# Kernel tuning notes

Measured on AMD Instinct MI355X. Metric: run time of the kernel, lower is better.

## Reference

```python
import jax, jax.numpy as jnp
import numpy as np

WH, WW = 16, 16          # window size
S = WH * WW              # tokens per window = 256
B = 128                  # batch of windows
E = 1024                 # embed_dim
H = 16                   # num_heads
D = E // H               # head_dim = 64


def _swin_rel_index():
    # Swin-style relative position index, identical to the torch buffer construction
    coords = np.stack(np.meshgrid(np.arange(WH), np.arange(WW), indexing='ij'))  # [2,WH,WW]
    cf = coords.reshape(2, -1)                         # [2, S]
    rel = cf[:, :, None] - cf[:, None, :]              # [2, S, S]
    rel = rel.transpose(1, 2, 0).copy()                # [S, S, 2]
    rel[..., 0] += WH - 1
    rel[..., 1] += WW - 1
    rel[..., 0] *= 2 * WW - 1
    return rel.sum(-1).astype(np.int32)                # [S, S] in [0, (2WH-1)(2WW-1))


def setup_inputs() -> dict:
    key = jax.random.key(0)
    ks = jax.random.split(key, 6)
    x = jax.random.normal(ks[0], (B, S, E), dtype=jnp.float32)
    qkv_w = jax.random.normal(ks[1], (3 * E, E), dtype=jnp.float32) * 0.02
    qkv_b = jax.random.normal(ks[2], (3 * E,), dtype=jnp.float32) * 0.02
    out_w = jax.random.normal(ks[3], (E, E), dtype=jnp.float32) * 0.02
    out_b = jax.random.normal(ks[4], (E,), dtype=jnp.float32) * 0.02
    bias_table = jax.random.normal(ks[5], ((2 * WH - 1) * (2 * WW - 1), H), dtype=jnp.float32) * 0.02
    rel_index = jnp.asarray(_swin_rel_index())
    return {"x": x, "qkv_w": qkv_w, "qkv_b": qkv_b, "out_w": out_w,
            "out_b": out_b, "bias_table": bias_table, "rel_index": rel_index,
            "x_ignored_": 0, "x_ignored_1_": 0}


def reference(x, qkv_w, qkv_b, out_w, out_b, bias_table, rel_index, x_ignored_, x_ignored_1_):
    b, s, e = x.shape
    h = bias_table.shape[-1]
    d = e // h
    # fused QKV projection
    qkv = x @ qkv_w.T + qkv_b                          # [b, s, 3e]
    qkv = qkv.reshape(b, s, 3, h, d)
    q, k, v = qkv[:, :, 0], qkv[:, :, 1], qkv[:, :, 2]  # [b, s, h, d]
    scale = d ** -0.5
    # learned relative position bias, [h, s, s]
    bias = bias_table[rel_index.reshape(-1)].reshape(s, s, h).transpose(2, 0, 1)
    scores = jnp.einsum('bqhd,bkhd->bhqk', q, k) * scale + bias[None]
    attn = jax.nn.softmax(scores, axis=-1)
    ctx = jnp.einsum('bhqk,bkhd->bqhd', attn, v).reshape(b, s, e)
    return ctx @ out_w.T + out_b
```

## Files before the change

### kernel.cpp

```cpp
#include <hip/hip_runtime.h>
#include <stdint.h>

#define BB 128
#define SS 256
#define EE 1024
#define HH 16
#define DD 64
#define MM (BB*SS)

#define LOG2E 1.44269504088896f

typedef __attribute__((ext_vector_type(8))) short bf16x8;
typedef __attribute__((ext_vector_type(4))) float f32x4;

__device__ __forceinline__ unsigned short f2bf(float f) {
  union { float f; unsigned int u; } c; c.f = f;
  unsigned int u = c.u;
  u += 0x7fffu + ((u >> 16) & 1u);
  return (unsigned short)(u >> 16);
}

__device__ __forceinline__ float fast_exp2(float x) {
#if __has_builtin(__builtin_amdgcn_exp2f)
  return __builtin_amdgcn_exp2f(x);
#else
  return exp2f(x);
#endif
}

__device__ __forceinline__ float fast_rcp(float x) {
#if __has_builtin(__builtin_amdgcn_rcpf)
  return __builtin_amdgcn_rcpf(x);
#else
  return 1.0f / x;
#endif
}

__device__ __forceinline__ void gld16(const unsigned short* g, unsigned short* l) {
  __builtin_amdgcn_global_load_lds((__attribute__((address_space(1))) void*)(g),
                                   (__attribute__((address_space(3))) void*)(l), 16, 0, 0);
}

__global__ __launch_bounds__(256) void prep_kernel(const float4* __restrict__ x4,
                                                   const float4* __restrict__ qw,
                                                   const float4* __restrict__ ow,
                                                   const float* __restrict__ btab,
                                                   const int* __restrict__ ridx,
                                                   ushort4* __restrict__ xb,
                                                   ushort4* __restrict__ qwb,
                                                   ushort4* __restrict__ owb,
                                                   float* __restrict__ biasC) {
  const int NX = (MM * EE) / 4;
  const int NQ = (3 * EE * EE) / 4;
  const int NO = (EE * EE) / 4;
  const int NBIAS = HH * SS * SS;
  const int total = NX + NQ + NO + NBIAS;
  int stride = gridDim.x * blockDim.x;
  for (int i = blockIdx.x * blockDim.x + threadIdx.x; i < total; i += stride) {
    if (i < NX) {
      float4 v = x4[i];
      ushort4 r; r.x = f2bf(v.x); r.y = f2bf(v.y); r.z = f2bf(v.z); r.w = f2bf(v.w);
      xb[i] = r;
    } else if (i < NX + NQ) {
      int t = i - NX;
      float4 v = qw[t];
      ushort4 r; r.x = f2bf(v.x); r.y = f2bf(v.y); r.z = f2bf(v.z); r.w = f2bf(v.w);
      qwb[t] = r;
    } else if (i < NX + NQ + NO) {
      int t = i - (NX + NQ);
      float4 v = ow[t];
      ushort4 r; r.x = f2bf(v.x); r.y = f2bf(v.y); r.z = f2bf(v.z); r.w = f2bf(v.w);
      owb[t] = r;
    } else {
      int t = i - (NX + NQ + NO);
      int h   = t >> 16;
      int row = (t >> 8) & 255;
      int lo  = (t >> 4) & 15;
      int hi  = t & 15;
      int col = hi * 16 + lo;
      biasC[t] = btab[ridx[row * SS + col] * HH + h] * LOG2E;
    }
  }
}

__device__ __forceinline__ void gemm_mainloop(const unsigned short* __restrict__ A,
                                              const unsigned short* __restrict__ Bw,
                                              unsigned short* As, unsigned short* Bs,
                                              int row0, int col0, int K,
                                              f32x4 acc[4][4]) {
  const int tid = threadIdx.x;
  const int wave = tid >> 6, lane = tid & 63;
  const int wm = wave & 1, wn = wave >> 1;
  const int l15 = lane & 15, quad = lane >> 4;
  const int ldrow = lane >> 2, ldc = lane & 3;
  const int gsw = (ldc ^ ((ldrow >> 1) & 3)) * 8;
  const int rsw = (l15 >> 1) & 3;
  const unsigned short* agp0 = A + (size_t)(row0 + wave * 16 + ldrow) * K + gsw;
  const unsigned short* agp1 = A + (size_t)(row0 + (4 + wave) * 16 + ldrow) * K + gsw;
  const unsigned short* bgp0 = Bw + (size_t)(col0 + wave * 16 + ldrow) * K + gsw;
  const unsigned short* bgp1 = Bw + (size_t)(col0 + (4 + wave) * 16 + ldrow) * K + gsw;
  unsigned short* al0 = As + wave * 512;
  unsigned short* al1 = As + (4 + wave) * 512;
  unsigned short* bl0 = Bs + wave * 512;
  unsigned short* bl1 = Bs + (4 + wave) * 512;
  for (int k0 = 0; k0 < K; k0 += 32) {
    gld16(agp0 + k0, al0);
    gld16(agp1 + k0, al1);
    gld16(bgp0 + k0, bl0);
    gld16(bgp1 + k0, bl1);
    __syncthreads();
    bf16x8 af[4], bfm[4];
#pragma unroll
    for (int i = 0; i < 4; ++i)
      af[i] = *(const bf16x8*)(As + (wm * 64 + i * 16 + l15) * 32 + (quad ^ rsw) * 8);
#pragma unroll
    for (int j = 0; j < 4; ++j)
      bfm[j] = *(const bf16x8*)(Bs + (wn * 64 + j * 16 + l15) * 32 + (quad ^ rsw) * 8);
#pragma unroll
    for (int i = 0; i < 4; ++i)
#pragma unroll
      for (int j = 0; j < 4; ++j)
        acc[i][j] = __builtin_amdgcn_mfma_f32_16x16x32_bf16(af[i], bfm[j], acc[i][j], 0, 0, 0);
    __syncthreads();
  }
}

__global__ __launch_bounds__(256) void qkv_gemm(const unsigned short* __restrict__ A,
                                                const unsigned short* __restrict__ Bw,
                                                const float* __restrict__ bias,
                                                unsigned short* __restrict__ q,
                                                unsigned short* __restrict__ kx,
                                                unsigned short* __restrict__ vt) {
  __shared__ unsigned short As[128 * 32];
  __shared__ unsigned short Bs[128 * 32];
  const int tid = threadIdx.x;
  const int wave = tid >> 6, lane = tid & 63;
  const int wm = wave & 1, wn = wave >> 1;
  const int l15 = lane & 15, quad = lane >> 4;
  const int row0 = blockIdx.x * 128;
  const int col0 = blockIdx.y * 128;
  f32x4 acc[4][4];
#pragma unroll
  for (int i = 0; i < 4; ++i)
#pragma unroll
    for (int j = 0; j < 4; ++j) acc[i][j] = (f32x4){0.f, 0.f, 0.f, 0.f};
  gemm_mainloop(A, Bw, As, Bs, row0, col0, EE, acc);
  const int which = col0 >> 10;
  const float QS = 0.125f * LOG2E;
#pragma unroll
  for (int i = 0; i < 4; ++i) {
    const int mbase = row0 + wm * 64 + i * 16 + quad * 4;
    const int bb = mbase >> 8;
    const int s0 = mbase & 255;
#pragma unroll
    for (int j = 0; j < 4; ++j) {
      const int n = col0 + wn * 64 + j * 16 + l15;
      const int hn = (n >> 6) & 15;
      const int d = n & 63;
      const float bv = bias[n];
      if (which == 0) {
        size_t base = ((size_t)(bb * HH + hn) * SS + s0) * DD + d;
#pragma unroll
        for (int r = 0; r < 4; ++r)
          q[base + (size_t)r * DD] = f2bf((acc[i][j][r] + bv) * QS);
      } else if (which == 1) {
        size_t base = ((size_t)(bb * HH + hn) * SS + s0) * DD + d;
#pragma unroll
        for (int r = 0; r < 4; ++r)
          kx[base + (size_t)r * DD] = f2bf(acc[i][j][r] + bv);
      } else {
        size_t base = ((size_t)(bb * HH + hn) * DD + d) * SS + s0;
        ushort4 pk;
        pk.x = f2bf(acc[i][j][0] + bv);
        pk.y = f2bf(acc[i][j][1] + bv);
        pk.z = f2bf(acc[i][j][2] + bv);
        pk.w = f2bf(acc[i][j][3] + bv);
        *(ushort4*)(vt + base) = pk;
      }
    }
  }
}

__global__ __launch_bounds__(256) void attn_kernel(const unsigned short* __restrict__ q,
                                                   const unsigned short* __restrict__ kx,
                                                   const unsigned short* __restrict__ vt,
                                                   const float* __restrict__ biasC,
                                                   unsigned short* __restrict__ ctx) {
  __shared__ unsigned short Ks[256 * 64];
  __shared__ unsigned short P[4][16 * 256];
  const int tid = threadIdx.x;
  const int wave = tid >> 6, lane = tid & 63;
  const int l15 = lane & 15, quad = lane >> 4;
  const int swl = l15 & 7;
  const int bh = blockIdx.x;
  const int h = bh & 15;
  const int b_ = bh >> 4;
  const unsigned short* qp = q + (size_t)bh * SS * DD;
  const unsigned short* kp = kx + (size_t)bh * SS * DD;
  const unsigned short* vp = vt + (size_t)bh * SS * DD;

#pragma unroll
  for (int rr = 0; rr < 8; ++rr) {
    int gc = rr * 256 + tid;
    int row = gc >> 3, sc = gc & 7;
    int c = sc ^ (row & 7);
    gld16(kp + row * 64 + c * 8, Ks + (rr * 256 + wave * 64) * 8);
  }
  __syncthreads();

  unsigned short* Pw = &P[wave][0];
  for (int qblk = 0; qblk < 4; ++qblk) {
    const int qr0 = qblk * 64 + wave * 16;
    bf16x8 aq0 = *(const bf16x8*)(qp + (qr0 + l15) * DD + quad * 8);
    bf16x8 aq1 = *(const bf16x8*)(qp + (qr0 + l15) * DD + 32 + quad * 8);

    f32x4 sacc[16];
#pragma unroll
    for (int j = 0; j < 16; ++j) sacc[j] = (f32x4){0.f, 0.f, 0.f, 0.f};
#pragma unroll
    for (int j = 0; j < 16; ++j) {
      const unsigned short* krow = Ks + (j * 16 + l15) * 64;
      bf16x8 b0 = *(const bf16x8*)(krow + (quad ^ swl) * 8);
      bf16x8 b1 = *(const bf16x8*)(krow + ((4 + quad) ^ swl) * 8);
      sacc[j] = __builtin_amdgcn_mfma_f32_16x16x32_bf16(aq0, b0, sacc[j], 0, 0, 0);
      sacc[j] = __builtin_amdgcn_mfma_f32_16x16x32_bf16(aq1, b1, sacc[j], 0, 0, 0);
    }
#pragma unroll
    for (int r = 0; r < 4; ++r) {
      const int prow = quad * 4 + r;
      const float* bC = biasC + ((size_t)((h * 256 + qr0 + prow) * 16 + l15)) * 16;
      float4 bv0 = ((const float4*)bC)[0];
      float4 bv1 = ((const float4*)bC)[1];
      float4 bv2 = ((const float4*)bC)[2];
      float4 bv3 = ((const float4*)bC)[3];
      float bj[16] = {bv0.x, bv0.y, bv0.z, bv0.w, bv1.x, bv1.y, bv1.z, bv1.w,
                      bv2.x, bv2.y, bv2.z, bv2.w, bv3.x, bv3.y, bv3.z, bv3.w};
      float s = 0.f;
#pragma unroll
      for (int j = 0; j < 16; ++j) {
        float e = fast_exp2(sacc[j][r] + bj[j]);
        sacc[j][r] = e;
        s += e;
      }
#pragma unroll
      for (int m = 8; m >= 1; m >>= 1) s += __shfl_xor(s, m, 16);
      float rs = fast_rcp(s);
      const int psw = prow & 7;
#pragma unroll
      for (int j = 0; j < 16; ++j) {
        union { float f; unsigned int u; } cv; cv.f = sacc[j][r] * rs;
        unsigned short pb = (unsigned short)((cv.u + 0x8000u) >> 16);
        Pw[prow * 256 + (((2 * j + (l15 >> 3)) ^ psw) << 3) + swl] = pb;
      }
    }
    f32x4 cacc[4];
#pragma unroll
    for (int nt = 0; nt < 4; ++nt) cacc[nt] = (f32x4){0.f, 0.f, 0.f, 0.f};
#pragma unroll
    for (int kk = 0; kk < 8; ++kk) {
      bf16x8 a = *(const bf16x8*)(Pw + l15 * 256 + (((kk * 4 + quad) ^ swl) << 3));
#pragma unroll
      for (int nt = 0; nt < 4; ++nt) {
        bf16x8 b = *(const bf16x8*)(vp + (nt * 16 + l15) * SS + kk * 32 + quad * 8);
        cacc[nt] = __builtin_amdgcn_mfma_f32_16x16x32_bf16(a, b, cacc[nt], 0, 0, 0);
      }
    }
#pragma unroll
    for (int nt = 0; nt < 4; ++nt)
#pragma unroll
      for (int r = 0; r < 4; ++r)
        ctx[(size_t)(b_ * SS + qr0 + quad * 4 + r) * EE + h * DD + nt * 16 + l15] =
            f2bf(cacc[nt][r]);
  }
}

__global__ __launch_bounds__(256) void out_gemm(const unsigned short* __restrict__ A,
                                                const unsigned short* __restrict__ Bw,
                                                const float* __restrict__ bias,
                                                float* __restrict__ out) {
  __shared__ unsigned short As[128 * 32];
  __shared__ unsigned short Bs[128 * 32];
  const int tid = threadIdx.x;
  const int wave = tid >> 6, lane = tid & 63;
  const int wm = wave & 1, wn = wave >> 1;
  const int l15 = lane & 15, quad = lane >> 4;
  const int row0 = blockIdx.x * 128;
  const int col0 = blockIdx.y * 128;
  f32x4 acc[4][4];
#pragma unroll
  for (int i = 0; i < 4; ++i)
#pragma unroll
    for (int j = 0; j < 4; ++j) acc[i][j] = (f32x4){0.f, 0.f, 0.f, 0.f};
  gemm_mainloop(A, Bw, As, Bs, row0, col0, EE, acc);
#pragma unroll
  for (int i = 0; i < 4; ++i) {
    const int m0 = row0 + wm * 64 + i * 16 + quad * 4;
#pragma unroll
    for (int j = 0; j < 4; ++j) {
      const int n = col0 + wn * 64 + j * 16 + l15;
      const float bv = bias[n];
#pragma unroll
      for (int r = 0; r < 4; ++r)
        out[(size_t)(m0 + r) * EE + n] = acc[i][j][r] + bv;
    }
  }
}

#define WS_XCTX  ((size_t)0)
#define WS_QKVW  ((size_t)67108864)
#define WS_OUTW  ((size_t)73400320)
#define WS_BIAS  ((size_t)75497472)
#define WS_Q     ((size_t)79691776)
#define WS_K     ((size_t)146800640)
#define WS_VT    ((size_t)213909504)

extern "C" void kernel_launch(void* const* d_in, const int* in_sizes, int n_in,
                              void* d_out, int out_size, void* d_ws, size_t ws_size,
                              hipStream_t stream) {
  (void)in_sizes; (void)n_in; (void)out_size; (void)ws_size;
  const float* x      = (const float*)d_in[0];
  const float* qkv_w  = (const float*)d_in[1];
  const float* qkv_b  = (const float*)d_in[2];
  const float* out_w  = (const float*)d_in[3];
  const float* out_b  = (const float*)d_in[4];
  const float* btab   = (const float*)d_in[5];
  const int*   ridx   = (const int*)d_in[6];
  float* out = (float*)d_out;
  char* ws = (char*)d_ws;

  unsigned short* xctx  = (unsigned short*)(ws + WS_XCTX);
  unsigned short* qkvwb = (unsigned short*)(ws + WS_QKVW);
  unsigned short* outwb = (unsigned short*)(ws + WS_OUTW);
  float*          biasC = (float*)(ws + WS_BIAS);
  unsigned short* q     = (unsigned short*)(ws + WS_Q);
  unsigned short* k     = (unsigned short*)(ws + WS_K);
  unsigned short* vt    = (unsigned short*)(ws + WS_VT);

  prep_kernel<<<8192, 256, 0, stream>>>((const float4*)x, (const float4*)qkv_w,
                                        (const float4*)out_w, btab, ridx,
                                        (ushort4*)xctx, (ushort4*)qkvwb,
                                        (ushort4*)outwb, biasC);
  qkv_gemm<<<dim3(MM / 128, (3 * EE) / 128), 256, 0, stream>>>(xctx, qkvwb, qkv_b,
                                                               q, k, vt);
  attn_kernel<<<BB * HH, 256, 0, stream>>>(q, k, vt, biasC, xctx);
  out_gemm<<<dim3(MM / 128, EE / 128), 256, 0, stream>>>(xctx, outwb, out_b, out);
}
```

Measured before the change: 786.8 us.

## Deepen GEMM K-tile, restructure attention to transposed scores with register P and LDS V

The GEMM main loop now loads 64-wide K slices per barrier with an 8-way XOR swizzle, halving the number of synchronisation rounds at the cost of doubled LDS per block. The attention kernel computes transposed scores (K as A operand), keeps the bf16 probabilities in registers and redistributes them with shuffles instead of writing them through LDS. It also stages V into LDS, defers softmax normalisation to the output, and uses a plain row-major bias layout. The exp2/rcp helpers are switched from the AMDGCN builtins to standard library calls, which may cost some precision-speed tradeoff.

```diff
diff --git a/kernel.cpp b/kernel.cpp
--- a/kernel.cpp
+++ b/kernel.cpp
@@ -20,21 +20,8 @@
   return (unsigned short)(u >> 16);
 }
 
-__device__ __forceinline__ float fast_exp2(float x) {
-#if __has_builtin(__builtin_amdgcn_exp2f)
-  return __builtin_amdgcn_exp2f(x);
-#else
-  return exp2f(x);
-#endif
-}
-
-__device__ __forceinline__ float fast_rcp(float x) {
-#if __has_builtin(__builtin_amdgcn_rcpf)
-  return __builtin_amdgcn_rcpf(x);
-#else
-  return 1.0f / x;
-#endif
-}
+__device__ __forceinline__ float fast_exp2(float x) { return exp2f(x); }
+__device__ __forceinline__ float fast_rcp(float x) { return 1.0f / x; }
 
 __device__ __forceinline__ void gld16(const unsigned short* g, unsigned short* l) {
   __builtin_amdgcn_global_load_lds((__attribute__((address_space(1))) void*)(g),
@@ -49,7 +36,7 @@
                                                    ushort4* __restrict__ xb,
                                                    ushort4* __restrict__ qwb,
                                                    ushort4* __restrict__ owb,
-                                                   float* __restrict__ biasC) {
+                                                   float* __restrict__ biasm) {
   const int NX = (MM * EE) / 4;
   const int NQ = (3 * EE * EE) / 4;
   const int NO = (EE * EE) / 4;
@@ -73,12 +60,9 @@
       owb[t] = r;
     } else {
       int t = i - (NX + NQ + NO);
-      int h   = t >> 16;
-      int row = (t >> 8) & 255;
-      int lo  = (t >> 4) & 15;
-      int hi  = t & 15;
-      int col = hi * 16 + lo;
-      biasC[t] = btab[ridx[row * SS + col] * HH + h] * LOG2E;
+      int h = t >> 16;
+      int qk = t & 65535;
+      biasm[t] = btab[ridx[qk] * HH + h] * LOG2E;
     }
   }
 }
@@ -92,35 +76,41 @@
   const int wave = tid >> 6, lane = tid & 63;
   const int wm = wave & 1, wn = wave >> 1;
   const int l15 = lane & 15, quad = lane >> 4;
-  const int ldrow = lane >> 2, ldc = lane & 3;
-  const int gsw = (ldc ^ ((ldrow >> 1) & 3)) * 8;
-  const int rsw = (l15 >> 1) & 3;
-  const unsigned short* agp0 = A + (size_t)(row0 + wave * 16 + ldrow) * K + gsw;
-  const unsigned short* agp1 = A + (size_t)(row0 + (4 + wave) * 16 + ldrow) * K + gsw;
-  const unsigned short* bgp0 = Bw + (size_t)(col0 + wave * 16 + ldrow) * K + gsw;
-  const unsigned short* bgp1 = Bw + (size_t)(col0 + (4 + wave) * 16 + ldrow) * K + gsw;
-  unsigned short* al0 = As + wave * 512;
-  unsigned short* al1 = As + (4 + wave) * 512;
-  unsigned short* bl0 = Bs + wave * 512;
-  unsigned short* bl1 = Bs + (4 + wave) * 512;
-  for (int k0 = 0; k0 < K; k0 += 32) {
-    gld16(agp0 + k0, al0);
-    gld16(agp1 + k0, al1);
-    gld16(bgp0 + k0, bl0);
-    gld16(bgp1 + k0, bl1);
+  const int swl = l15 & 7;
+  const unsigned short* ap[4];
+  const unsigned short* bp[4];
+#pragma unroll
+  for (int p = 0; p < 4; ++p) {
+    int slot = p * 256 + tid;
+    int srow = slot >> 3;
+    int sgc = ((slot & 7) ^ (srow & 7)) * 8;
+    ap[p] = A + (size_t)(row0 + srow) * K + sgc;
+    bp[p] = Bw + (size_t)(col0 + srow) * K + sgc;
+  }
+  for (int k0 = 0; k0 < K; k0 += 64) {
+#pragma unroll
+    for (int p = 0; p < 4; ++p) {
+      gld16(ap[p] + k0, As + (p * 256 + wave * 64) * 8);
+      gld16(bp[p] + k0, Bs + (p * 256 + wave * 64) * 8);
+    }
     __syncthreads();
-    bf16x8 af[4], bfm[4];
-#pragma unroll
-    for (int i = 0; i < 4; ++i)
-      af[i] = *(const bf16x8*)(As + (wm * 64 + i * 16 + l15) * 32 + (quad ^ rsw) * 8);
-#pragma unroll
-    for (int j = 0; j < 4; ++j)
-      bfm[j] = *(const bf16x8*)(Bs + (wn * 64 + j * 16 + l15) * 32 + (quad ^ rsw) * 8);
-#pragma unroll
-    for (int i = 0; i < 4; ++i)
+#pragma unroll
+    for (int ks = 0; ks < 2; ++ks) {
+      bf16x8 af[4], bfm[4];
+#pragma unroll
+      for (int i = 0; i < 4; ++i)
+        af[i] = *(const bf16x8*)(As + (wm * 64 + i * 16 + l15) * 64 +
+                                 (((ks * 4 + quad) ^ swl)) * 8);
 #pragma unroll
       for (int j = 0; j < 4; ++j)
-        acc[i][j] = __builtin_amdgcn_mfma_f32_16x16x32_bf16(af[i], bfm[j], acc[i][j], 0, 0, 0);
+        bfm[j] = *(const bf16x8*)(Bs + (wn * 64 + j * 16 + l15) * 64 +
+                                  (((ks * 4 + quad) ^ swl)) * 8);
+#pragma unroll
+      for (int i = 0; i < 4; ++i)
+#pragma unroll
+        for (int j = 0; j < 4; ++j)
+          acc[i][j] = __builtin_amdgcn_mfma_f32_16x16x32_bf16(af[i], bfm[j], acc[i][j], 0, 0, 0);
+    }
     __syncthreads();
   }
 }
@@ -131,8 +121,8 @@
                                                 unsigned short* __restrict__ q,
                                                 unsigned short* __restrict__ kx,
                                                 unsigned short* __restrict__ vt) {
-  __shared__ unsigned short As[128 * 32];
-  __shared__ unsigned short Bs[128 * 32];
+  __shared__ unsigned short As[128 * 64];
+  __shared__ unsigned short Bs[128 * 64];
   const int tid = threadIdx.x;
   const int wave = tid >> 6, lane = tid & 63;
   const int wm = wave & 1, wn = wave >> 1;
@@ -184,10 +174,10 @@
 __global__ __launch_bounds__(256) void attn_kernel(const unsigned short* __restrict__ q,
                                                    const unsigned short* __restrict__ kx,
                                                    const unsigned short* __restrict__ vt,
-                                                   const float* __restrict__ biasC,
+                                                   const float* __restrict__ biasm,
                                                    unsigned short* __restrict__ ctx) {
   __shared__ unsigned short Ks[256 * 64];
-  __shared__ unsigned short P[4][16 * 256];
+  __shared__ unsigned short Vs[64 * 256];
   const int tid = threadIdx.x;
   const int wave = tid >> 6, lane = tid & 63;
   const int l15 = lane & 15, quad = lane >> 4;
@@ -197,7 +187,7 @@
   const int b_ = bh >> 4;
   const unsigned short* qp = q + (size_t)bh * SS * DD;
   const unsigned short* kp = kx + (size_t)bh * SS * DD;
-  const unsigned short* vp = vt + (size_t)bh * SS * DD;
+  const unsigned short* vp = vt + (size_t)bh * DD * SS;
 
 #pragma unroll
   for (int rr = 0; rr < 8; ++rr) {
@@ -206,71 +196,90 @@
     int c = sc ^ (row & 7);
     gld16(kp + row * 64 + c * 8, Ks + (rr * 256 + wave * 64) * 8);
   }
+#pragma unroll
+  for (int rr = 0; rr < 8; ++rr) {
+    int slot = rr * 256 + tid;
+    int row = slot >> 5, sc = slot & 31;
+    int c = (sc & 24) | ((sc & 7) ^ (row & 7));
+    gld16(vp + row * 256 + c * 8, Vs + (rr * 256 + wave * 64) * 8);
+  }
   __syncthreads();
 
-  unsigned short* Pw = &P[wave][0];
+  const int src_lo = ((quad & 1) << 5) + l15;
+  const int src_hi = src_lo + 16;
+  const int hiSel = quad >> 1;
+
   for (int qblk = 0; qblk < 4; ++qblk) {
     const int qr0 = qblk * 64 + wave * 16;
-    bf16x8 aq0 = *(const bf16x8*)(qp + (qr0 + l15) * DD + quad * 8);
-    bf16x8 aq1 = *(const bf16x8*)(qp + (qr0 + l15) * DD + 32 + quad * 8);
+    bf16x8 bq0 = *(const bf16x8*)(qp + (qr0 + l15) * DD + quad * 8);
+    bf16x8 bq1 = *(const bf16x8*)(qp + (qr0 + l15) * DD + 32 + quad * 8);
 
     f32x4 sacc[16];
 #pragma unroll
-    for (int j = 0; j < 16; ++j) sacc[j] = (f32x4){0.f, 0.f, 0.f, 0.f};
-#pragma unroll
-    for (int j = 0; j < 16; ++j) {
-      const unsigned short* krow = Ks + (j * 16 + l15) * 64;
-      bf16x8 b0 = *(const bf16x8*)(krow + (quad ^ swl) * 8);
-      bf16x8 b1 = *(const bf16x8*)(krow + ((4 + quad) ^ swl) * 8);
-      sacc[j] = __builtin_amdgcn_mfma_f32_16x16x32_bf16(aq0, b0, sacc[j], 0, 0, 0);
-      sacc[j] = __builtin_amdgcn_mfma_f32_16x16x32_bf16(aq1, b1, sacc[j], 0, 0, 0);
-    }
-#pragma unroll
-    for (int r = 0; r < 4; ++r) {
-      const int prow = quad * 4 + r;
-      const float* bC = biasC + ((size_t)((h * 256 + qr0 + prow) * 16 + l15)) * 16;
-      float4 bv0 = ((const float4*)bC)[0];
-      float4 bv1 = ((const float4*)bC)[1];
-      float4 bv2 = ((const float4*)bC)[2];
-      float4 bv3 = ((const float4*)bC)[3];
-      float bj[16] = {bv0.x, bv0.y, bv0.z, bv0.w, bv1.x, bv1.y, bv1.z, bv1.w,
-                      bv2.x, bv2.y, bv2.z, bv2.w, bv3.x, bv3.y, bv3.z, bv3.w};
-      float s = 0.f;
-#pragma unroll
-      for (int j = 0; j < 16; ++j) {
-        float e = fast_exp2(sacc[j][r] + bj[j]);
-        sacc[j][r] = e;
-        s += e;
+    for (int jt = 0; jt < 16; ++jt) sacc[jt] = (f32x4){0.f, 0.f, 0.f, 0.f};
+#pragma unroll
+    for (int jt = 0; jt < 16; ++jt) {
+      const unsigned short* krow = Ks + (jt * 16 + l15) * 64;
+      bf16x8 a0 = *(const bf16x8*)(krow + (quad ^ swl) * 8);
+      bf16x8 a1 = *(const bf16x8*)(krow + ((4 + quad) ^ swl) * 8);
+      sacc[jt] = __builtin_amdgcn_mfma_f32_16x16x32_bf16(a0, bq0, sacc[jt], 0, 0, 0);
+      sacc[jt] = __builtin_amdgcn_mfma_f32_16x16x32_bf16(a1, bq1, sacc[jt], 0, 0, 0);
+    }
+    const float* bbp = biasm + ((size_t)(h * 256 + qr0 + l15)) * 256;
+    float s = 0.f;
+    uint2 pk[16];
+#pragma unroll
+    for (int jt = 0; jt < 16; ++jt) {
+      float4 bv = *(const float4*)(bbp + jt * 16 + quad * 4);
+      float e0 = fast_exp2(sacc[jt][0] + bv.x);
+      float e1 = fast_exp2(sacc[jt][1] + bv.y);
+      float e2 = fast_exp2(sacc[jt][2] + bv.z);
+      float e3 = fast_exp2(sacc[jt][3] + bv.w);
+      s += (e0 + e1) + (e2 + e3);
+      union { float f; unsigned u; } u0, u1, u2, u3;
+      u0.f = e0; u1.f = e1; u2.f = e2; u3.f = e3;
+      pk[jt].x = ((u0.u + 0x8000u) >> 16) | ((u1.u + 0x8000u) & 0xffff0000u);
+      pk[jt].y = ((u2.u + 0x8000u) >> 16) | ((u3.u + 0x8000u) & 0xffff0000u);
+    }
+    s += __shfl_xor(s, 16);
+    s += __shfl_xor(s, 32);
+    float rs = fast_rcp(s);
+
+    f32x4 cacc[4];
+#pragma unroll
+    for (int nt = 0; nt < 4; ++nt) cacc[nt] = (f32x4){0.f, 0.f, 0.f, 0.f};
+#pragma unroll
+    for (int kk = 0; kk < 8; ++kk) {
+      unsigned lex = __shfl((int)pk[2 * kk].x, src_lo);
+      unsigned ley = __shfl((int)pk[2 * kk].y, src_lo);
+      unsigned lox = __shfl((int)pk[2 * kk + 1].x, src_lo);
+      unsigned loy = __shfl((int)pk[2 * kk + 1].y, src_lo);
+      unsigned hex_ = __shfl((int)pk[2 * kk].x, src_hi);
+      unsigned hey = __shfl((int)pk[2 * kk].y, src_hi);
+      unsigned hox = __shfl((int)pk[2 * kk + 1].x, src_hi);
+      unsigned hoy = __shfl((int)pk[2 * kk + 1].y, src_hi);
+      union { unsigned u[4]; bf16x8 v; } af;
+      af.u[0] = hiSel ? lox : lex;
+      af.u[1] = hiSel ? loy : ley;
+      af.u[2] = hiSel ? hox : hex_;
+      af.u[3] = hiSel ? hoy : hey;
+#pragma unroll
+      for (int nt = 0; nt < 4; ++nt) {
+        int c = kk * 4 + quad;
+        int cp = (c & 24) | ((c & 7) ^ swl);
+        bf16x8 b = *(const bf16x8*)(Vs + (nt * 16 + l15) * 256 + cp * 8);
+        cacc[nt] = __builtin_amdgcn_mfma_f32_16x16x32_bf16(af.v, b, cacc[nt], 0, 0, 0);
       }
-#pragma unroll
-      for (int m = 8; m >= 1; m >>= 1) s += __shfl_xor(s, m, 16);
-      float rs = fast_rcp(s);
-      const int psw = prow & 7;
-#pragma unroll
-      for (int j = 0; j < 16; ++j) {
-        union { float f; unsigned int u; } cv; cv.f = sacc[j][r] * rs;
-        unsigned short pb = (unsigned short)((cv.u + 0x8000u) >> 16);
-        Pw[prow * 256 + (((2 * j + (l15 >> 3)) ^ psw) << 3) + swl] = pb;
-      }
-    }
-    f32x4 cacc[4];
-#pragma unroll
-    for (int nt = 0; nt < 4; ++nt) cacc[nt] = (f32x4){0.f, 0.f, 0.f, 0.f};
-#pragma unroll
-    for (int kk = 0; kk < 8; ++kk) {
-      bf16x8 a = *(const bf16x8*)(Pw + l15 * 256 + (((kk * 4 + quad) ^ swl) << 3));
-#pragma unroll
-      for (int nt = 0; nt < 4; ++nt) {
-        bf16x8 b = *(const bf16x8*)(vp + (nt * 16 + l15) * SS + kk * 32 + quad * 8);
-        cacc[nt] = __builtin_amdgcn_mfma_f32_16x16x32_bf16(a, b, cacc[nt], 0, 0, 0);
-      }
-    }
+    }
+    float rsr[4];
+#pragma unroll
+    for (int r = 0; r < 4; ++r) rsr[r] = __shfl(rs, quad * 4 + r);
 #pragma unroll
     for (int nt = 0; nt < 4; ++nt)
 #pragma unroll
       for (int r = 0; r < 4; ++r)
         ctx[(size_t)(b_ * SS + qr0 + quad * 4 + r) * EE + h * DD + nt * 16 + l15] =
-            f2bf(cacc[nt][r]);
+            f2bf(cacc[nt][r] * rsr[r]);
   }
 }
 
@@ -278,8 +287,8 @@
                                                 const unsigned short* __restrict__ Bw,
                                                 const float* __restrict__ bias,
                                                 float* __restrict__ out) {
-  __shared__ unsigned short As[128 * 32];
-  __shared__ unsigned short Bs[128 * 32];
+  __shared__ unsigned short As[128 * 64];
+  __shared__ unsigned short Bs[128 * 64];
   const int tid = threadIdx.x;
   const int wave = tid >> 6, lane = tid & 63;
   const int wm = wave & 1, wn = wave >> 1;
@@ -331,7 +340,7 @@
   unsigned short* xctx  = (unsigned short*)(ws + WS_XCTX);
   unsigned short* qkvwb = (unsigned short*)(ws + WS_QKVW);
   unsigned short* outwb = (unsigned short*)(ws + WS_OUTW);
-  float*          biasC = (float*)(ws + WS_BIAS);
+  float*          biasm = (float*)(ws + WS_BIAS);
   unsigned short* q     = (unsigned short*)(ws + WS_Q);
   unsigned short* k     = (unsigned short*)(ws + WS_K);
   unsigned short* vt    = (unsigned short*)(ws + WS_VT);
@@ -339,9 +348,9 @@
   prep_kernel<<<8192, 256, 0, stream>>>((const float4*)x, (const float4*)qkv_w,
                                         (const float4*)out_w, btab, ridx,
                                         (ushort4*)xctx, (ushort4*)qkvwb,
-                                        (ushort4*)outwb, biasC);
+                                        (ushort4*)outwb, biasm);
   qkv_gemm<<<dim3(MM / 128, (3 * EE) / 128), 256, 0, stream>>>(xctx, qkvwb, qkv_b,
                                                                q, k, vt);
-  attn_kernel<<<BB * HH, 256, 0, stream>>>(q, k, vt, biasC, xctx);
+  attn_kernel<<<BB * HH, 256, 0, stream>>>(q, k, vt, biasm, xctx);
   out_gemm<<<dim3(MM / 128, EE / 128), 256, 0, stream>>>(xctx, outwb, out_b, out);
 }
```

Result: slower. 853.6 us (+8.5%).
